# Kernel tuning notes

Hardware: AMD Instinct MI355X
Metric: run time of the kernel (lower is better)

## Reference

```python
import jax, jax.numpy as jnp
import numpy as np

N_NODES = 50000
N_EDGES = 800000
IN_DIM = 128
HIDDEN = 128


def setup_inputs() -> dict:
    key = jax.random.key(0)
    ks = jax.random.split(key, 6)
    x = jax.random.normal(ks[0], (N_NODES, IN_DIM), dtype=jnp.float32)
    edge_index = jax.random.randint(ks[1], (2, N_EDGES), 0, N_NODES, dtype=jnp.int32)
    W1 = jax.random.normal(ks[2], (IN_DIM, HIDDEN), dtype=jnp.float32) * 0.05
    b1 = jnp.zeros((HIDDEN,), dtype=jnp.float32)
    W2 = jax.random.normal(ks[3], (HIDDEN, HIDDEN), dtype=jnp.float32) * 0.05
    b2 = jnp.zeros((HIDDEN,), dtype=jnp.float32)
    return {"x": x, "edge_index": edge_index, "W1": W1, "b1": b1, "W2": W2, "b2": b2}


def _gcn_conv(x, W, b, src, dst, norm, n):
    # PyG GCNConv: linear transform, then normalized sum-aggregate, then bias.
    h = x @ W                                  # [N, H]
    msg = h[src] * norm[:, None]               # gather + scale  [E+N, H]
    out = jax.ops.segment_sum(msg, dst, num_segments=n)
    return out + b


def reference(x, edge_index, W1, b1, W2, b2):
    n = x.shape[0]
    # add self-loops (GCNConv default add_self_loops=True)
    loops = jnp.arange(n, dtype=edge_index.dtype)
    src = jnp.concatenate([edge_index[0], loops])
    dst = jnp.concatenate([edge_index[1], loops])
    # symmetric normalization: deg over destination nodes (edge_weight = 1)
    deg = jax.ops.segment_sum(jnp.ones(src.shape, dtype=x.dtype), dst, num_segments=n)
    dinv = jax.lax.rsqrt(deg)                  # deg >= 1 because of self-loops
    norm = dinv[src] * dinv[dst]               # [E+N]
    h = jax.nn.relu(_gcn_conv(x, W1, b1, src, dst, norm, n))
    return _gcn_conv(h, W2, b2, src, dst, norm, n)
```

## Files before the change

### kernel.cpp

```cpp
#include <hip/hip_runtime.h>

#define N_NODES 50000
#define N_EDGES 800000
#define DIM 128
#define CHUNK 4096
#define GRID 196
#define SEG_CAP 6144
#define GEMM_BLOCKS 391
#define GA 316
#define GB (GEMM_BLOCKS - GA)

typedef __attribute__((ext_vector_type(8))) short bf16x8;
typedef __attribute__((ext_vector_type(4))) float f32x4;


__device__ inline unsigned rne_bf16(float f) {
    unsigned u = __float_as_uint(f);
    return (u + 0x7FFFu + ((u >> 16) & 1u)) >> 16;
}
__device__ inline unsigned pk_bf16(float a, float b) {
    return rne_bf16(a) | (rne_bf16(b) << 16);
}
__device__ inline float bf_lo(unsigned u) { return __uint_as_float(u << 16); }
__device__ inline float bf_hi(unsigned u) { return __uint_as_float(u & 0xFFFF0000u); }


__device__ void fragw_build(const float* __restrict__ W, uint4* __restrict__ fh,
                            uint4* __restrict__ fl, int slot) {
    const int lane = slot & 63, tile = slot >> 6;
    const int c = tile >> 2, q = tile & 3;
    const int k0 = q * 32 + ((lane >> 4) << 3);
    const int col = c * 16 + (lane & 15);
    unsigned h[8], l[8];
#pragma unroll
    for (int j = 0; j < 8; ++j) {
        float w = W[(size_t)(k0 + j) * DIM + col];
        unsigned hb = rne_bf16(w);
        h[j] = hb;
        l[j] = rne_bf16(w - __uint_as_float(hb << 16));
    }
    uint4 uh, ul;
    uh.x = h[0] | (h[1] << 16); uh.y = h[2] | (h[3] << 16);
    uh.z = h[4] | (h[5] << 16); uh.w = h[6] | (h[7] << 16);
    ul.x = l[0] | (l[1] << 16); ul.y = l[2] | (l[3] << 16);
    ul.z = l[4] | (l[5] << 16); ul.w = l[6] | (l[7] << 16);
    fh[slot] = uh;
    fl[slot] = ul;
}


__global__ __launch_bounds__(256) void chunk_hist_fragw(const int* __restrict__ dst,
                                                        int* __restrict__ chist,
                                                        const float* __restrict__ W1,
                                                        const float* __restrict__ W2,
                                                        uint4* f1h, uint4* f1l,
                                                        uint4* f2h, uint4* f2l) {
    const int bid = blockIdx.x;
    if (bid < GRID) {
        __shared__ int hist[256];
        const int t = threadIdx.x;
        const int eb = bid * CHUNK;
        const int cnt = min(CHUNK, N_EDGES - eb);
        hist[t] = 0;
        __syncthreads();
        for (int i = t; i < cnt; i += 256)
            atomicAdd(&hist[dst[eb + i] >> 8], 1);
        __syncthreads();
        chist[bid * 256 + t] = hist[t];
    } else {
        const int b2 = bid - GRID;
        const int slot = (b2 & 7) * 256 + threadIdx.x;
        if (b2 < 8) fragw_build(W1, f1h, f1l, slot);
        else        fragw_build(W2, f2h, f2l, slot);
    }
}


__device__ void gemm_body(const float* __restrict__ X,
                          const uint4* __restrict__ fWh,
                          const uint4* __restrict__ fWl,
                          uint2* __restrict__ O, int gb, char* smem) {
    const int t = threadIdx.x;

    {
        uint4* s4 = (uint4*)smem;
        for (int i = t; i < 2048; i += 256) {
            s4[i] = fWh[i];
            s4[2048 + i] = fWl[i];
        }
    }
    __syncthreads();

    const int w = t >> 6, lane = t & 63;
    const int lrow = lane & 15, lgrp = lane >> 4;
    const int rbase = gb * 128;

    bf16x8 Ah[2][4], Al[2][4];
#pragma unroll
    for (int m = 0; m < 2; ++m) {
        const int r = rbase + w * 32 + m * 16 + lrow;
        const bool ok = (r < N_NODES);
        const float4* xp = (const float4*)(X + (size_t)r * DIM + lgrp * 8);
#pragma unroll
        for (int q = 0; q < 4; ++q) {
            float4 a0 = ok ? xp[q * 8]     : make_float4(0.f, 0.f, 0.f, 0.f);
            float4 a1 = ok ? xp[q * 8 + 1] : make_float4(0.f, 0.f, 0.f, 0.f);
            float f[8] = {a0.x, a0.y, a0.z, a0.w, a1.x, a1.y, a1.z, a1.w};
            bf16x8 hi, lo;
#pragma unroll
            for (int j = 0; j < 8; ++j) {
                unsigned hb = rne_bf16(f[j]);
                hi[j] = (short)hb;
                lo[j] = (short)rne_bf16(f[j] - __uint_as_float(hb << 16));
            }
            Ah[m][q] = hi;
            Al[m][q] = lo;
        }
    }

    f32x4 acc[2][8];
#pragma unroll
    for (int m = 0; m < 2; ++m)
#pragma unroll
        for (int c = 0; c < 8; ++c)
            acc[m][c] = (f32x4){0.f, 0.f, 0.f, 0.f};

    const bf16x8* Bh = (const bf16x8*)smem;
    const bf16x8* Bl = (const bf16x8*)(smem + 32768);
#pragma unroll
    for (int c = 0; c < 8; ++c) {
#pragma unroll
        for (int q = 0; q < 4; ++q) {
            bf16x8 bh = Bh[(c * 4 + q) * 64 + lane];
            bf16x8 bl = Bl[(c * 4 + q) * 64 + lane];
#pragma unroll
            for (int m = 0; m < 2; ++m) {
                acc[m][c] = __builtin_amdgcn_mfma_f32_16x16x32_bf16(Ah[m][q], bh, acc[m][c], 0, 0, 0);
                acc[m][c] = __builtin_amdgcn_mfma_f32_16x16x32_bf16(Al[m][q], bh, acc[m][c], 0, 0, 0);
                acc[m][c] = __builtin_amdgcn_mfma_f32_16x16x32_bf16(Ah[m][q], bl, acc[m][c], 0, 0, 0);
            }
        }
    }

    __syncthreads();
    float* Lf = (float*)smem;
#pragma unroll
    for (int m = 0; m < 2; ++m)
#pragma unroll
        for (int c = 0; c < 8; ++c)
#pragma unroll
            for (int rg = 0; rg < 4; ++rg)
                Lf[(w * 32 + m * 16 + lgrp * 4 + rg) * DIM + c * 16 + lrow] = acc[m][c][rg];
    __syncthreads();

    const float4* Lf4 = (const float4*)smem;
    for (int idx = t; idx < 4096; idx += 256) {
        const int row = idx >> 5, s = idx & 31;
        const int gr = rbase + row;
        if (gr < N_NODES) {
            float4 v = Lf4[idx];
            uint2 o;
            o.x = pk_bf16(v.x, v.y);
            o.y = pk_bf16(v.z, v.w);
            O[(size_t)gr * 32 + s] = o;
        }
    }
}


__device__ void sort_scatter_body(const int* __restrict__ src,
                                  const int* __restrict__ dst,
                                  const int* __restrict__ chist,
                                  unsigned* __restrict__ sorted,
                                  int* __restrict__ bbase_g,
                                  int bid, char* smem) {
    int* hist  = (int*)smem;
    int* sc    = hist + 256;
    int* lbase = sc + 256;
    int* lcur  = lbase + 256;
    int* gbase = lcur + 256;
    unsigned* sl = (unsigned*)(smem + 5 * 1024);

    const int t = threadIdx.x;
    const int eb = bid * CHUNK;
    const int cnt = min(CHUNK, N_EDGES - eb);

    int sum = 0, myoff = 0;
    for (int c = 0; c < GRID; ++c) {
        int v = chist[c * 256 + t];
        if (c == bid) myoff = sum;
        sum += v;
    }
    hist[t] = chist[bid * 256 + t];
    sc[t] = sum;
    __syncthreads();
    for (int off = 1; off < 256; off <<= 1) {
        int u = (t >= off) ? sc[t - off] : 0;
        __syncthreads();
        sc[t] += u;
        __syncthreads();
    }
    gbase[t] = (sc[t] - sum) + myoff;
    if (bid == 0) bbase_g[t] = sc[t] - sum;
    __syncthreads();

    sc[t] = hist[t];
    __syncthreads();
    for (int off = 1; off < 256; off <<= 1) {
        int u = (t >= off) ? sc[t - off] : 0;
        __syncthreads();
        sc[t] += u;
        __syncthreads();
    }
    int ex = sc[t] - hist[t];
    lbase[t] = ex;
    lcur[t] = ex;
    __syncthreads();

    for (int i = t; i < cnt; i += 256) {
        int s = src[eb + i], d = dst[eb + i];
        int b = d >> 8;
        int p = atomicAdd(&lcur[b], 1);
        sl[p] = ((unsigned)b << 24) | ((unsigned)(d & 255) << 16) | (unsigned)s;
    }
    __syncthreads();
    for (int i = t; i < cnt; i += 256) {
        unsigned rec = sl[i];
        int b = rec >> 24;
        sorted[gbase[b] + (i - lbase[b])] = rec;
    }
}


__device__ void csr_build_body(const unsigned* __restrict__ sorted,
                               const int* __restrict__ bbase,
                               int* __restrict__ rowptr,
                               float* __restrict__ dinv,
                               int* __restrict__ csr,
                               int k, char* smem) {
    int* hist = (int*)smem;
    int* sc   = hist + 256;
    int* lcur = sc + 256;
    int* seg  = (int*)(smem + 3 * 1024);

    const int t = threadIdx.x;
    const int base = bbase[k];
    const int cntk = ((k == 255) ? N_EDGES : bbase[k + 1]) - base;
    if (k == 0 && t == 0) rowptr[N_NODES] = N_EDGES;

    hist[t] = 0;
    __syncthreads();
    for (int i = t; i < cntk; i += 256)
        atomicAdd(&hist[(sorted[base + i] >> 16) & 255], 1);
    __syncthreads();

    const int node = (k << 8) + t;
    const int dv = hist[t];
    if (node < N_NODES) dinv[node] = rsqrtf((float)dv + 1.0f);

    sc[t] = dv;
    __syncthreads();
    for (int off = 1; off < 256; off <<= 1) {
        int u = (t >= off) ? sc[t - off] : 0;
        __syncthreads();
        sc[t] += u;
        __syncthreads();
    }
    int ex = sc[t] - dv;
    if (node < N_NODES) rowptr[node] = base + ex;
    lcur[t] = ex;
    __syncthreads();

    if (cntk <= SEG_CAP) {
        for (int i = t; i < cntk; i += 256) {
            unsigned rec = sorted[base + i];
            int p = atomicAdd(&lcur[(rec >> 16) & 255], 1);
            seg[p] = (int)(rec & 0xFFFFu);
        }
        __syncthreads();
        for (int i = t; i < cntk; i += 256)
            csr[base + i] = seg[i];
    } else {
        for (int i = t; i < cntk; i += 256) {
            unsigned rec = sorted[base + i];
            int p = atomicAdd(&lcur[(rec >> 16) & 255], 1);
            csr[base + p] = (int)(rec & 0xFFFFu);
        }
    }
}


__global__ __launch_bounds__(256, 2) void sort_gemm(const int* __restrict__ src,
                                                    const int* __restrict__ dst,
                                                    const int* __restrict__ chist,
                                                    unsigned* __restrict__ sorted,
                                                    int* __restrict__ bbase_g,
                                                    const float* __restrict__ X,
                                                    const uint4* __restrict__ fWh,
                                                    const uint4* __restrict__ fWl,
                                                    uint2* __restrict__ O) {
    __shared__ __align__(16) char smem[65536];
    if (blockIdx.x < GRID)
        sort_scatter_body(src, dst, chist, sorted, bbase_g, blockIdx.x, smem);
    else
        gemm_body(X, fWh, fWl, O, blockIdx.x - GRID, smem);
}

__global__ __launch_bounds__(256, 2) void csr_gemm(const unsigned* __restrict__ sorted,
                                                   const int* __restrict__ bbase,
                                                   int* __restrict__ rowptr,
                                                   float* __restrict__ dinv,
                                                   int* __restrict__ csr,
                                                   const float* __restrict__ X,
                                                   const uint4* __restrict__ fWh,
                                                   const uint4* __restrict__ fWl,
                                                   uint2* __restrict__ O) {
    __shared__ __align__(16) char smem[65536];
    if (blockIdx.x < GRID)
        csr_build_body(sorted, bbase, rowptr, dinv, csr, blockIdx.x, smem);
    else
        gemm_body(X, fWh, fWl, O, blockIdx.x - GRID + GA, smem);
}


__device__ inline float4 agg_node(int node, const uint2* __restrict__ H2,
                                  const int* __restrict__ rowptr,
                                  const int* __restrict__ csr,
                                  const float* __restrict__ dinv,
                                  const float4* __restrict__ b4, int relu) {
    const int lane = threadIdx.x & 63;
    const int half = lane >> 5;
    const int col  = lane & 31;

    const float dn = dinv[node];
    float4 acc = make_float4(0.f, 0.f, 0.f, 0.f);
    if (half == 0) {
        uint2 v = H2[(size_t)node * 32 + col];
        acc.x = dn * bf_lo(v.x); acc.y = dn * bf_hi(v.x);
        acc.z = dn * bf_lo(v.y); acc.w = dn * bf_hi(v.y);
    }

    int j = rowptr[node];
    const int end = rowptr[node + 1];

#define ACC(v, ds) do { \
        acc.x = fmaf((ds), bf_lo((v).x), acc.x); \
        acc.y = fmaf((ds), bf_hi((v).x), acc.y); \
        acc.z = fmaf((ds), bf_lo((v).y), acc.z); \
        acc.w = fmaf((ds), bf_hi((v).y), acc.w); } while (0)

    for (; j + 16 <= end; j += 16) {
        int s0 = csr[j +  0 + half], s1 = csr[j +  2 + half];
        int s2 = csr[j +  4 + half], s3 = csr[j +  6 + half];
        int s4 = csr[j +  8 + half], s5 = csr[j + 10 + half];
        int s6 = csr[j + 12 + half], s7 = csr[j + 14 + half];
        uint2 v0 = H2[(size_t)s0 * 32 + col]; float d0 = dinv[s0];
        uint2 v1 = H2[(size_t)s1 * 32 + col]; float d1 = dinv[s1];
        uint2 v2 = H2[(size_t)s2 * 32 + col]; float d2 = dinv[s2];
        uint2 v3 = H2[(size_t)s3 * 32 + col]; float d3 = dinv[s3];
        uint2 v4 = H2[(size_t)s4 * 32 + col]; float d4 = dinv[s4];
        uint2 v5 = H2[(size_t)s5 * 32 + col]; float d5 = dinv[s5];
        uint2 v6 = H2[(size_t)s6 * 32 + col]; float d6 = dinv[s6];
        uint2 v7 = H2[(size_t)s7 * 32 + col]; float d7 = dinv[s7];
        ACC(v0, d0); ACC(v1, d1); ACC(v2, d2); ACC(v3, d3);
        ACC(v4, d4); ACC(v5, d5); ACC(v6, d6); ACC(v7, d7);
    }
    if (j + 8 <= end) {
        int s0 = csr[j + half], s1 = csr[j + 2 + half];
        int s2 = csr[j + 4 + half], s3 = csr[j + 6 + half];
        uint2 v0 = H2[(size_t)s0 * 32 + col]; float d0 = dinv[s0];
        uint2 v1 = H2[(size_t)s1 * 32 + col]; float d1 = dinv[s1];
        uint2 v2 = H2[(size_t)s2 * 32 + col]; float d2 = dinv[s2];
        uint2 v3 = H2[(size_t)s3 * 32 + col]; float d3 = dinv[s3];
        ACC(v0, d0); ACC(v1, d1); ACC(v2, d2); ACC(v3, d3);
        j += 8;
    }
    if (j + 4 <= end) {
        int s0 = csr[j + half], s1 = csr[j + 2 + half];
        uint2 v0 = H2[(size_t)s0 * 32 + col]; float d0 = dinv[s0];
        uint2 v1 = H2[(size_t)s1 * 32 + col]; float d1 = dinv[s1];
        ACC(v0, d0); ACC(v1, d1);
        j += 4;
    }
    if (j + 2 <= end) {
        int s = csr[j + half];
        uint2 v = H2[(size_t)s * 32 + col]; float d0 = dinv[s];
        ACC(v, d0);
        j += 2;
    }
    if (j < end && half == 0) {
        int s = csr[j];
        uint2 v = H2[(size_t)s * 32 + col]; float d0 = dinv[s];
        ACC(v, d0);
    }
#undef ACC

    acc.x += __shfl_xor(acc.x, 32, 64);
    acc.y += __shfl_xor(acc.y, 32, 64);
    acc.z += __shfl_xor(acc.z, 32, 64);
    acc.w += __shfl_xor(acc.w, 32, 64);

    float4 o = make_float4(0.f, 0.f, 0.f, 0.f);
    if (half == 0) {
        float4 bb = b4[col];
        o.x = acc.x * dn + bb.x;
        o.y = acc.y * dn + bb.y;
        o.z = acc.z * dn + bb.z;
        o.w = acc.w * dn + bb.w;
        if (relu) {
            o.x = fmaxf(o.x, 0.f); o.y = fmaxf(o.y, 0.f);
            o.z = fmaxf(o.z, 0.f); o.w = fmaxf(o.w, 0.f);
        }
    }
    return o;
}


__global__ __launch_bounds__(256) void aggregate_h1(const uint2* __restrict__ H2,
                                                    const int* __restrict__ rowptr,
                                                    const int* __restrict__ csr,
                                                    const float* __restrict__ dinv,
                                                    const float4* __restrict__ b4,
                                                    uint2* __restrict__ h1h,
                                                    uint2* __restrict__ h1l) {
    int node = blockIdx.x * 4 + (threadIdx.x >> 6);
    if (node >= N_NODES) return;
    float4 o = agg_node(node, H2, rowptr, csr, dinv, b4, 1);
    const int lane = threadIdx.x & 63;
    if (lane < 32) {
        unsigned hx = rne_bf16(o.x), hy = rne_bf16(o.y);
        unsigned hz = rne_bf16(o.z), hw = rne_bf16(o.w);
        unsigned lx = rne_bf16(o.x - __uint_as_float(hx << 16));
        unsigned ly = rne_bf16(o.y - __uint_as_float(hy << 16));
        unsigned lz = rne_bf16(o.z - __uint_as_float(hz << 16));
        unsigned lw = rne_bf16(o.w - __uint_as_float(hw << 16));
        uint2 hv; hv.x = hx | (hy << 16); hv.y = hz | (hw << 16);
        uint2 lv; lv.x = lx | (ly << 16); lv.y = lz | (lw << 16);
        h1h[(size_t)node * 32 + lane] = hv;
        h1l[(size_t)node * 32 + lane] = lv;
    }
}


__global__ __launch_bounds__(256) void aggregate_out(const uint2* __restrict__ H2,
                                                     const int* __restrict__ rowptr,
                                                     const int* __restrict__ csr,
                                                     const float* __restrict__ dinv,
                                                     const float4* __restrict__ b4,
                                                     float4* __restrict__ out) {
    int node = blockIdx.x * 4 + (threadIdx.x >> 6);
    if (node >= N_NODES) return;
    float4 o = agg_node(node, H2, rowptr, csr, dinv, b4, 0);
    const int lane = threadIdx.x & 63;
    if (lane < 32) out[(size_t)node * 32 + lane] = o;
}


__global__ __launch_bounds__(256, 2) void gemm_xw2(const uint2* __restrict__ h1h,
                                                   const uint2* __restrict__ h1l,
                                                   const uint4* __restrict__ fWh,
                                                   const uint4* __restrict__ fWl,
                                                   uint2* __restrict__ O) {
    __shared__ __align__(16) char smem[65536];
    const int t = threadIdx.x;

    {
        uint4* s4 = (uint4*)smem;
        for (int i = t; i < 2048; i += 256) {
            s4[i] = fWh[i];
            s4[2048 + i] = fWl[i];
        }
    }
    __syncthreads();

    const int w = t >> 6, lane = t & 63;
    const int lrow = lane & 15, lgrp = lane >> 4;
    const int rbase = blockIdx.x * 128;

    bf16x8 Ah[2][4], Al[2][4];
    const bf16x8 zz = (bf16x8){0,0,0,0,0,0,0,0};
#pragma unroll
    for (int m = 0; m < 2; ++m) {
        const int r = rbase + w * 32 + m * 16 + lrow;
        const bool ok = (r < N_NODES);
        const uint2* ph = h1h + (size_t)r * 32 + lgrp * 2;
        const uint2* pl = h1l + (size_t)r * 32 + lgrp * 2;
#pragma unroll
        for (int q = 0; q < 4; ++q) {
            Ah[m][q] = ok ? *(const bf16x8*)(ph + q * 8) : zz;
            Al[m][q] = ok ? *(const bf16x8*)(pl + q * 8) : zz;
        }
    }

    f32x4 acc[2][8];
#pragma unroll
    for (int m = 0; m < 2; ++m)
#pragma unroll
        for (int c = 0; c < 8; ++c)
            acc[m][c] = (f32x4){0.f, 0.f, 0.f, 0.f};

    const bf16x8* Bh = (const bf16x8*)smem;
    const bf16x8* Bl = (const bf16x8*)(smem + 32768);
#pragma unroll
    for (int c = 0; c < 8; ++c) {
#pragma unroll
        for (int q = 0; q < 4; ++q) {
            bf16x8 bh = Bh[(c * 4 + q) * 64 + lane];
            bf16x8 bl = Bl[(c * 4 + q) * 64 + lane];
#pragma unroll
            for (int m = 0; m < 2; ++m) {
                acc[m][c] = __builtin_amdgcn_mfma_f32_16x16x32_bf16(Ah[m][q], bh, acc[m][c], 0, 0, 0);
                acc[m][c] = __builtin_amdgcn_mfma_f32_16x16x32_bf16(Al[m][q], bh, acc[m][c], 0, 0, 0);
                acc[m][c] = __builtin_amdgcn_mfma_f32_16x16x32_bf16(Ah[m][q], bl, acc[m][c], 0, 0, 0);
            }
        }
    }

    __syncthreads();
    float* Lf = (float*)smem;
#pragma unroll
    for (int m = 0; m < 2; ++m)
#pragma unroll
        for (int c = 0; c < 8; ++c)
#pragma unroll
            for (int rg = 0; rg < 4; ++rg)
                Lf[(w * 32 + m * 16 + lgrp * 4 + rg) * DIM + c * 16 + lrow] = acc[m][c][rg];
    __syncthreads();

    const float4* Lf4 = (const float4*)smem;
    for (int idx = t; idx < 4096; idx += 256) {
        const int row = idx >> 5, s = idx & 31;
        const int gr = rbase + row;
        if (gr < N_NODES) {
            float4 v = Lf4[idx];
            uint2 o;
            o.x = pk_bf16(v.x, v.y);
            o.y = pk_bf16(v.z, v.w);
            O[(size_t)gr * 32 + s] = o;
        }
    }
}


extern "C" void kernel_launch(void* const* d_in, const int* in_sizes, int n_in,
                              void* d_out, int out_size, void* d_ws, size_t ws_size,
                              hipStream_t stream) {
    const float* x  = (const float*)d_in[0];
    const int*   ei = (const int*)d_in[1];
    const float* W1 = (const float*)d_in[2];
    const float* b1 = (const float*)d_in[3];
    const float* W2 = (const float*)d_in[4];
    const float* b2 = (const float*)d_in[5];
    float* out = (float*)d_out;

    const int* src = ei;
    const int* dst = ei + N_EDGES;

    char* p = (char*)d_ws;
    int*      chist  = (int*)p;              p += GRID * 256 * 4;
    float*    dinv   = (float*)p;            p += ((N_NODES * 4 + 1023) & ~1023);
    int*      rowptr = (int*)p;              p += (((N_NODES + 1) * 4 + 1023) & ~1023);
    unsigned* sorted = (unsigned*)p;         p += ((N_EDGES * 4 + 1023) & ~1023);
    int*      csr    = (int*)p;              p += ((N_EDGES * 4 + 1023) & ~1023);
    int*      bbase  = (int*)p;              p += 1024;
    uint4*    f1h    = (uint4*)p;            p += 32768;
    uint4*    f1l    = (uint4*)p;            p += 32768;
    uint4*    f2h    = (uint4*)p;            p += 32768;
    uint4*    f2l    = (uint4*)p;            p += 32768;
    uint2*    hp     = (uint2*)p;            p += (size_t)N_NODES * DIM * 2;
    uint2*    h1h    = (uint2*)p;            p += (size_t)N_NODES * DIM * 2;
    uint2*    h1l    = (uint2*)p;            p += (size_t)N_NODES * DIM * 2;
    uint2*    hp2    = (uint2*)p;

    const int aggBlocks = (N_NODES + 3) / 4;

    chunk_hist_fragw<<<GRID + 16, 256, 0, stream>>>(dst, chist, W1, W2,
                                                    f1h, f1l, f2h, f2l);
    sort_gemm<<<GRID + GA, 256, 0, stream>>>(src, dst, chist, sorted, bbase,
                                             x, f1h, f1l, hp);
    csr_gemm<<<GRID + GB, 256, 0, stream>>>(sorted, bbase, rowptr, dinv, csr,
                                            x, f1h, f1l, hp);

    aggregate_h1<<<aggBlocks, 256, 0, stream>>>(hp, rowptr, csr, dinv,
                                                (const float4*)b1, h1h, h1l);

    gemm_xw2<<<GEMM_BLOCKS, 256, 0, stream>>>(h1h, h1l, f2h, f2l, hp2);

    aggregate_out<<<aggBlocks, 256, 0, stream>>>(hp2, rowptr, csr, dinv,
                                                 (const float4*)b2, (float4*)out);
}
```

Before: 209.1 us.

## Split aggregation feature dimension into four slices with 8-way edge parallelism

Each wavefront now handles one 32-column slice of a node's 128 features, with 8 lane groups processing different edges in parallel instead of 2 halves. The grid grows fourfold, with slice-major block ordering, so there are more waves in flight to hide gather latency and the tail handling becomes a single predicated step. The cost is four times the csr/dinv index reads, smaller 64-byte row segments per gather, and an extra shuffle reduction stage. Each slice pass may also lose L2 locality across the whole graph.

After: 296.4 us. 1.42x slower.

```diff
diff --git a/kernel.cpp b/kernel.cpp
--- a/kernel.cpp
+++ b/kernel.cpp
@@ -9,6 +9,7 @@
 #define GEMM_BLOCKS 391
 #define GA 316
 #define GB (GEMM_BLOCKS - GA)
+#define AGG_NB 12500
 
 typedef __attribute__((ext_vector_type(8))) short bf16x8;
 typedef __attribute__((ext_vector_type(4))) float f32x4;
@@ -323,19 +324,20 @@
 }
 
 
-__device__ inline float4 agg_node(int node, const uint2* __restrict__ H2,
-                                  const int* __restrict__ rowptr,
-                                  const int* __restrict__ csr,
-                                  const float* __restrict__ dinv,
-                                  const float4* __restrict__ b4, int relu) {
+__device__ inline float4 agg_node_slice(int node, int slice,
+                                        const uint2* __restrict__ H2,
+                                        const int* __restrict__ rowptr,
+                                        const int* __restrict__ csr,
+                                        const float* __restrict__ dinv,
+                                        const float4* __restrict__ b4, int relu) {
     const int lane = threadIdx.x & 63;
-    const int half = lane >> 5;
-    const int col  = lane & 31;
+    const int g    = lane >> 3;
+    const int idx  = slice * 8 + (lane & 7);
 
     const float dn = dinv[node];
     float4 acc = make_float4(0.f, 0.f, 0.f, 0.f);
-    if (half == 0) {
-        uint2 v = H2[(size_t)node * 32 + col];
+    if (g == 0) {
+        uint2 v = H2[(size_t)node * 32 + idx];
         acc.x = dn * bf_lo(v.x); acc.y = dn * bf_hi(v.x);
         acc.z = dn * bf_lo(v.y); acc.w = dn * bf_hi(v.y);
     }
@@ -350,59 +352,42 @@
         acc.w = fmaf((ds), bf_hi((v).y), acc.w); } while (0)
 
     for (; j + 16 <= end; j += 16) {
-        int s0 = csr[j +  0 + half], s1 = csr[j +  2 + half];
-        int s2 = csr[j +  4 + half], s3 = csr[j +  6 + half];
-        int s4 = csr[j +  8 + half], s5 = csr[j + 10 + half];
-        int s6 = csr[j + 12 + half], s7 = csr[j + 14 + half];
-        uint2 v0 = H2[(size_t)s0 * 32 + col]; float d0 = dinv[s0];
-        uint2 v1 = H2[(size_t)s1 * 32 + col]; float d1 = dinv[s1];
-        uint2 v2 = H2[(size_t)s2 * 32 + col]; float d2 = dinv[s2];
-        uint2 v3 = H2[(size_t)s3 * 32 + col]; float d3 = dinv[s3];
-        uint2 v4 = H2[(size_t)s4 * 32 + col]; float d4 = dinv[s4];
-        uint2 v5 = H2[(size_t)s5 * 32 + col]; float d5 = dinv[s5];
-        uint2 v6 = H2[(size_t)s6 * 32 + col]; float d6 = dinv[s6];
-        uint2 v7 = H2[(size_t)s7 * 32 + col]; float d7 = dinv[s7];
-        ACC(v0, d0); ACC(v1, d1); ACC(v2, d2); ACC(v3, d3);
-        ACC(v4, d4); ACC(v5, d5); ACC(v6, d6); ACC(v7, d7);
+        int s0 = csr[j + g];
+        int s1 = csr[j + 8 + g];
+        uint2 v0 = H2[(size_t)s0 * 32 + idx]; float d0 = dinv[s0];
+        uint2 v1 = H2[(size_t)s1 * 32 + idx]; float d1 = dinv[s1];
+        ACC(v0, d0); ACC(v1, d1);
     }
     if (j + 8 <= end) {
-        int s0 = csr[j + half], s1 = csr[j + 2 + half];
-        int s2 = csr[j + 4 + half], s3 = csr[j + 6 + half];
-        uint2 v0 = H2[(size_t)s0 * 32 + col]; float d0 = dinv[s0];
-        uint2 v1 = H2[(size_t)s1 * 32 + col]; float d1 = dinv[s1];
-        uint2 v2 = H2[(size_t)s2 * 32 + col]; float d2 = dinv[s2];
-        uint2 v3 = H2[(size_t)s3 * 32 + col]; float d3 = dinv[s3];
-        ACC(v0, d0); ACC(v1, d1); ACC(v2, d2); ACC(v3, d3);
+        int s = csr[j + g];
+        uint2 v = H2[(size_t)s * 32 + idx]; float d = dinv[s];
+        ACC(v, d);
         j += 8;
     }
-    if (j + 4 <= end) {
-        int s0 = csr[j + half], s1 = csr[j + 2 + half];
-        uint2 v0 = H2[(size_t)s0 * 32 + col]; float d0 = dinv[s0];
-        uint2 v1 = H2[(size_t)s1 * 32 + col]; float d1 = dinv[s1];
-        ACC(v0, d0); ACC(v1, d1);
-        j += 4;
-    }
-    if (j + 2 <= end) {
-        int s = csr[j + half];
-        uint2 v = H2[(size_t)s * 32 + col]; float d0 = dinv[s];
-        ACC(v, d0);
-        j += 2;
-    }
-    if (j < end && half == 0) {
-        int s = csr[j];
-        uint2 v = H2[(size_t)s * 32 + col]; float d0 = dinv[s];
-        ACC(v, d0);
+    const int rem = end - j;
+    if (g < rem) {
+        int s = csr[j + g];
+        uint2 v = H2[(size_t)s * 32 + idx]; float d = dinv[s];
+        ACC(v, d);
     }
 #undef ACC
 
+    acc.x += __shfl_xor(acc.x,  8, 64);
+    acc.y += __shfl_xor(acc.y,  8, 64);
+    acc.z += __shfl_xor(acc.z,  8, 64);
+    acc.w += __shfl_xor(acc.w,  8, 64);
+    acc.x += __shfl_xor(acc.x, 16, 64);
+    acc.y += __shfl_xor(acc.y, 16, 64);
+    acc.z += __shfl_xor(acc.z, 16, 64);
+    acc.w += __shfl_xor(acc.w, 16, 64);
     acc.x += __shfl_xor(acc.x, 32, 64);
     acc.y += __shfl_xor(acc.y, 32, 64);
     acc.z += __shfl_xor(acc.z, 32, 64);
     acc.w += __shfl_xor(acc.w, 32, 64);
 
     float4 o = make_float4(0.f, 0.f, 0.f, 0.f);
-    if (half == 0) {
-        float4 bb = b4[col];
+    if (lane < 8) {
+        float4 bb = b4[idx];
         o.x = acc.x * dn + bb.x;
         o.y = acc.y * dn + bb.y;
         o.z = acc.z * dn + bb.z;
@@ -423,11 +408,14 @@
                                                     const float4* __restrict__ b4,
                                                     uint2* __restrict__ h1h,
                                                     uint2* __restrict__ h1l) {
-    int node = blockIdx.x * 4 + (threadIdx.x >> 6);
+    const int slice = blockIdx.x / AGG_NB;
+    const int nb    = blockIdx.x % AGG_NB;
+    const int node  = nb * 4 + (threadIdx.x >> 6);
     if (node >= N_NODES) return;
-    float4 o = agg_node(node, H2, rowptr, csr, dinv, b4, 1);
+    float4 o = agg_node_slice(node, slice, H2, rowptr, csr, dinv, b4, 1);
     const int lane = threadIdx.x & 63;
-    if (lane < 32) {
+    if (lane < 8) {
+        const int idx = slice * 8 + lane;
         unsigned hx = rne_bf16(o.x), hy = rne_bf16(o.y);
         unsigned hz = rne_bf16(o.z), hw = rne_bf16(o.w);
         unsigned lx = rne_bf16(o.x - __uint_as_float(hx << 16));
@@ -436,8 +424,8 @@
         unsigned lw = rne_bf16(o.w - __uint_as_float(hw << 16));
         uint2 hv; hv.x = hx | (hy << 16); hv.y = hz | (hw << 16);
         uint2 lv; lv.x = lx | (ly << 16); lv.y = lz | (lw << 16);
-        h1h[(size_t)node * 32 + lane] = hv;
-        h1l[(size_t)node * 32 + lane] = lv;
+        h1h[(size_t)node * 32 + idx] = hv;
+        h1l[(size_t)node * 32 + idx] = lv;
     }
 }
 
@@ -448,11 +436,13 @@
                                                      const float* __restrict__ dinv,
                                                      const float4* __restrict__ b4,
                                                      float4* __restrict__ out) {
-    int node = blockIdx.x * 4 + (threadIdx.x >> 6);
+    const int slice = blockIdx.x / AGG_NB;
+    const int nb    = blockIdx.x % AGG_NB;
+    const int node  = nb * 4 + (threadIdx.x >> 6);
     if (node >= N_NODES) return;
-    float4 o = agg_node(node, H2, rowptr, csr, dinv, b4, 0);
+    float4 o = agg_node_slice(node, slice, H2, rowptr, csr, dinv, b4, 0);
     const int lane = threadIdx.x & 63;
-    if (lane < 32) out[(size_t)node * 32 + lane] = o;
+    if (lane < 8) out[(size_t)node * 32 + slice * 8 + lane] = o;
 }
 
 
@@ -572,8 +562,6 @@
     uint2*    h1l    = (uint2*)p;            p += (size_t)N_NODES * DIM * 2;
     uint2*    hp2    = (uint2*)p;
 
-    const int aggBlocks = (N_NODES + 3) / 4;
-
     chunk_hist_fragw<<<GRID + 16, 256, 0, stream>>>(dst, chist, W1, W2,
                                                     f1h, f1l, f2h, f2l);
     sort_gemm<<<GRID + GA, 256, 0, stream>>>(src, dst, chist, sorted, bbase,
@@ -581,11 +569,11 @@
     csr_gemm<<<GRID + GB, 256, 0, stream>>>(sorted, bbase, rowptr, dinv, csr,
                                             x, f1h, f1l, hp);
 
-    aggregate_h1<<<aggBlocks, 256, 0, stream>>>(hp, rowptr, csr, dinv,
-                                                (const float4*)b1, h1h, h1l);
+    aggregate_h1<<<4 * AGG_NB, 256, 0, stream>>>(hp, rowptr, csr, dinv,
+                                                 (const float4*)b1, h1h, h1l);
 
     gemm_xw2<<<GEMM_BLOCKS, 256, 0, stream>>>(h1h, h1l, f2h, f2l, hp2);
 
-    aggregate_out<<<aggBlocks, 256, 0, stream>>>(hp2, rowptr, csr, dinv,
-                                                 (const float4*)b2, (float4*)out);
-}
+    aggregate_out<<<4 * AGG_NB, 256, 0, stream>>>(hp2, rowptr, csr, dinv,
+                                                  (const float4*)b2, (float4*)out);
+}
```

## Widen aggregation gathers to 16-byte loads and prescale layer-2 input by dinv

Applied to the files above, without the earlier changes.

The aggregation kernels now have each wavefront split into four quarter-groups of 16 lanes that each load a full 128-bit slice per neighbor row, instead of two halves loading 64-bit slices. The layer-1 output is additionally multiplied by dinv before being stored, so the second aggregation drops its per-neighbor dinv gather and does plain adds. The aim is fewer, wider memory transactions and less random dinv traffic. The trade-off is an extra shuffle reduction stage and more registers per lane. Moving the dinv scale before the GEMM relies on it being linear, which holds but changes rounding slightly.

Result: faster. 203.5 us (-2.7%).

```diff
diff --git a/kernel.cpp b/kernel.cpp
--- a/kernel.cpp
+++ b/kernel.cpp
@@ -323,97 +323,17 @@
 }
 
 
-__device__ inline float4 agg_node(int node, const uint2* __restrict__ H2,
-                                  const int* __restrict__ rowptr,
-                                  const int* __restrict__ csr,
-                                  const float* __restrict__ dinv,
-                                  const float4* __restrict__ b4, int relu) {
-    const int lane = threadIdx.x & 63;
-    const int half = lane >> 5;
-    const int col  = lane & 31;
-
-    const float dn = dinv[node];
-    float4 acc = make_float4(0.f, 0.f, 0.f, 0.f);
-    if (half == 0) {
-        uint2 v = H2[(size_t)node * 32 + col];
-        acc.x = dn * bf_lo(v.x); acc.y = dn * bf_hi(v.x);
-        acc.z = dn * bf_lo(v.y); acc.w = dn * bf_hi(v.y);
-    }
-
-    int j = rowptr[node];
-    const int end = rowptr[node + 1];
-
-#define ACC(v, ds) do { \
-        acc.x = fmaf((ds), bf_lo((v).x), acc.x); \
-        acc.y = fmaf((ds), bf_hi((v).x), acc.y); \
-        acc.z = fmaf((ds), bf_lo((v).y), acc.z); \
-        acc.w = fmaf((ds), bf_hi((v).y), acc.w); } while (0)
-
-    for (; j + 16 <= end; j += 16) {
-        int s0 = csr[j +  0 + half], s1 = csr[j +  2 + half];
-        int s2 = csr[j +  4 + half], s3 = csr[j +  6 + half];
-        int s4 = csr[j +  8 + half], s5 = csr[j + 10 + half];
-        int s6 = csr[j + 12 + half], s7 = csr[j + 14 + half];
-        uint2 v0 = H2[(size_t)s0 * 32 + col]; float d0 = dinv[s0];
-        uint2 v1 = H2[(size_t)s1 * 32 + col]; float d1 = dinv[s1];
-        uint2 v2 = H2[(size_t)s2 * 32 + col]; float d2 = dinv[s2];
-        uint2 v3 = H2[(size_t)s3 * 32 + col]; float d3 = dinv[s3];
-        uint2 v4 = H2[(size_t)s4 * 32 + col]; float d4 = dinv[s4];
-        uint2 v5 = H2[(size_t)s5 * 32 + col]; float d5 = dinv[s5];
-        uint2 v6 = H2[(size_t)s6 * 32 + col]; float d6 = dinv[s6];
-        uint2 v7 = H2[(size_t)s7 * 32 + col]; float d7 = dinv[s7];
-        ACC(v0, d0); ACC(v1, d1); ACC(v2, d2); ACC(v3, d3);
-        ACC(v4, d4); ACC(v5, d5); ACC(v6, d6); ACC(v7, d7);
-    }
-    if (j + 8 <= end) {
-        int s0 = csr[j + half], s1 = csr[j + 2 + half];
-        int s2 = csr[j + 4 + half], s3 = csr[j + 6 + half];
-        uint2 v0 = H2[(size_t)s0 * 32 + col]; float d0 = dinv[s0];
-        uint2 v1 = H2[(size_t)s1 * 32 + col]; float d1 = dinv[s1];
-        uint2 v2 = H2[(size_t)s2 * 32 + col]; float d2 = dinv[s2];
-        uint2 v3 = H2[(size_t)s3 * 32 + col]; float d3 = dinv[s3];
-        ACC(v0, d0); ACC(v1, d1); ACC(v2, d2); ACC(v3, d3);
-        j += 8;
-    }
-    if (j + 4 <= end) {
-        int s0 = csr[j + half], s1 = csr[j + 2 + half];
-        uint2 v0 = H2[(size_t)s0 * 32 + col]; float d0 = dinv[s0];
-        uint2 v1 = H2[(size_t)s1 * 32 + col]; float d1 = dinv[s1];
-        ACC(v0, d0); ACC(v1, d1);
-        j += 4;
-    }
-    if (j + 2 <= end) {
-        int s = csr[j + half];
-        uint2 v = H2[(size_t)s * 32 + col]; float d0 = dinv[s];
-        ACC(v, d0);
-        j += 2;
-    }
-    if (j < end && half == 0) {
-        int s = csr[j];
-        uint2 v = H2[(size_t)s * 32 + col]; float d0 = dinv[s];
-        ACC(v, d0);
-    }
-#undef ACC
-
-    acc.x += __shfl_xor(acc.x, 32, 64);
-    acc.y += __shfl_xor(acc.y, 32, 64);
-    acc.z += __shfl_xor(acc.z, 32, 64);
-    acc.w += __shfl_xor(acc.w, 32, 64);
-
-    float4 o = make_float4(0.f, 0.f, 0.f, 0.f);
-    if (half == 0) {
-        float4 bb = b4[col];
-        o.x = acc.x * dn + bb.x;
-        o.y = acc.y * dn + bb.y;
-        o.z = acc.z * dn + bb.z;
-        o.w = acc.w * dn + bb.w;
-        if (relu) {
-            o.x = fmaxf(o.x, 0.f); o.y = fmaxf(o.y, 0.f);
-            o.z = fmaxf(o.z, 0.f); o.w = fmaxf(o.w, 0.f);
-        }
-    }
-    return o;
-}
+#define ACC8_D(v, d) do { \
+        a0 = fmaf((d), bf_lo((v).x), a0); a1 = fmaf((d), bf_hi((v).x), a1); \
+        a2 = fmaf((d), bf_lo((v).y), a2); a3 = fmaf((d), bf_hi((v).y), a3); \
+        a4 = fmaf((d), bf_lo((v).z), a4); a5 = fmaf((d), bf_hi((v).z), a5); \
+        a6 = fmaf((d), bf_lo((v).w), a6); a7 = fmaf((d), bf_hi((v).w), a7); } while (0)
+
+#define ACC8_P(v) do { \
+        a0 += bf_lo((v).x); a1 += bf_hi((v).x); \
+        a2 += bf_lo((v).y); a3 += bf_hi((v).y); \
+        a4 += bf_lo((v).z); a5 += bf_hi((v).z); \
+        a6 += bf_lo((v).w); a7 += bf_hi((v).w); } while (0)
 
 
 __global__ __launch_bounds__(256) void aggregate_h1(const uint2* __restrict__ H2,
@@ -421,23 +341,75 @@
                                                     const int* __restrict__ csr,
                                                     const float* __restrict__ dinv,
                                                     const float4* __restrict__ b4,
-                                                    uint2* __restrict__ h1h,
-                                                    uint2* __restrict__ h1l) {
-    int node = blockIdx.x * 4 + (threadIdx.x >> 6);
+                                                    uint4* __restrict__ h1h4,
+                                                    uint4* __restrict__ h1l4) {
+    const int node = blockIdx.x * 4 + (threadIdx.x >> 6);
     if (node >= N_NODES) return;
-    float4 o = agg_node(node, H2, rowptr, csr, dinv, b4, 1);
     const int lane = threadIdx.x & 63;
-    if (lane < 32) {
-        unsigned hx = rne_bf16(o.x), hy = rne_bf16(o.y);
-        unsigned hz = rne_bf16(o.z), hw = rne_bf16(o.w);
-        unsigned lx = rne_bf16(o.x - __uint_as_float(hx << 16));
-        unsigned ly = rne_bf16(o.y - __uint_as_float(hy << 16));
-        unsigned lz = rne_bf16(o.z - __uint_as_float(hz << 16));
-        unsigned lw = rne_bf16(o.w - __uint_as_float(hw << 16));
-        uint2 hv; hv.x = hx | (hy << 16); hv.y = hz | (hw << 16);
-        uint2 lv; lv.x = lx | (ly << 16); lv.y = lz | (lw << 16);
-        h1h[(size_t)node * 32 + lane] = hv;
-        h1l[(size_t)node * 32 + lane] = lv;
+    const int q = lane >> 4, l16 = lane & 15;
+    const uint4* H4 = (const uint4*)H2;
+
+    const float dn = dinv[node];
+    float a0 = 0.f, a1 = 0.f, a2 = 0.f, a3 = 0.f,
+          a4 = 0.f, a5 = 0.f, a6 = 0.f, a7 = 0.f;
+    if (q == 0) {
+        uint4 v = H4[(size_t)node * 16 + l16];
+        ACC8_D(v, dn);
+    }
+
+    int j = rowptr[node];
+    const int end = rowptr[node + 1];
+    for (; j + 8 <= end; j += 8) {
+        int s0 = csr[j + q], s1 = csr[j + 4 + q];
+        uint4 v0 = H4[(size_t)s0 * 16 + l16]; float d0 = dinv[s0];
+        uint4 v1 = H4[(size_t)s1 * 16 + l16]; float d1 = dinv[s1];
+        ACC8_D(v0, d0); ACC8_D(v1, d1);
+    }
+    if (j + 4 <= end) {
+        int s = csr[j + q];
+        uint4 v = H4[(size_t)s * 16 + l16]; float d = dinv[s];
+        ACC8_D(v, d);
+        j += 4;
+    }
+    if (q < end - j) {
+        int s = csr[j + q];
+        uint4 v = H4[(size_t)s * 16 + l16]; float d = dinv[s];
+        ACC8_D(v, d);
+    }
+
+    a0 += __shfl_xor(a0, 16, 64); a1 += __shfl_xor(a1, 16, 64);
+    a2 += __shfl_xor(a2, 16, 64); a3 += __shfl_xor(a3, 16, 64);
+    a4 += __shfl_xor(a4, 16, 64); a5 += __shfl_xor(a5, 16, 64);
+    a6 += __shfl_xor(a6, 16, 64); a7 += __shfl_xor(a7, 16, 64);
+    a0 += __shfl_xor(a0, 32, 64); a1 += __shfl_xor(a1, 32, 64);
+    a2 += __shfl_xor(a2, 32, 64); a3 += __shfl_xor(a3, 32, 64);
+    a4 += __shfl_xor(a4, 32, 64); a5 += __shfl_xor(a5, 32, 64);
+    a6 += __shfl_xor(a6, 32, 64); a7 += __shfl_xor(a7, 32, 64);
+
+    if (lane < 16) {
+        float4 bbA = b4[l16 * 2], bbB = b4[l16 * 2 + 1];
+        float o0 = fmaxf(a0 * dn + bbA.x, 0.f), o1 = fmaxf(a1 * dn + bbA.y, 0.f);
+        float o2 = fmaxf(a2 * dn + bbA.z, 0.f), o3 = fmaxf(a3 * dn + bbA.w, 0.f);
+        float o4 = fmaxf(a4 * dn + bbB.x, 0.f), o5 = fmaxf(a5 * dn + bbB.y, 0.f);
+        float o6 = fmaxf(a6 * dn + bbB.z, 0.f), o7 = fmaxf(a7 * dn + bbB.w, 0.f);
+        o0 *= dn; o1 *= dn; o2 *= dn; o3 *= dn;
+        o4 *= dn; o5 *= dn; o6 *= dn; o7 *= dn;
+        unsigned h0 = rne_bf16(o0), h1 = rne_bf16(o1), h2 = rne_bf16(o2), h3 = rne_bf16(o3);
+        unsigned h4 = rne_bf16(o4), h5 = rne_bf16(o5), h6 = rne_bf16(o6), h7 = rne_bf16(o7);
+        uint4 hv;
+        hv.x = h0 | (h1 << 16); hv.y = h2 | (h3 << 16);
+        hv.z = h4 | (h5 << 16); hv.w = h6 | (h7 << 16);
+        uint4 lv;
+        lv.x = rne_bf16(o0 - __uint_as_float(h0 << 16)) |
+               (rne_bf16(o1 - __uint_as_float(h1 << 16)) << 16);
+        lv.y = rne_bf16(o2 - __uint_as_float(h2 << 16)) |
+               (rne_bf16(o3 - __uint_as_float(h3 << 16)) << 16);
+        lv.z = rne_bf16(o4 - __uint_as_float(h4 << 16)) |
+               (rne_bf16(o5 - __uint_as_float(h5 << 16)) << 16);
+        lv.w = rne_bf16(o6 - __uint_as_float(h6 << 16)) |
+               (rne_bf16(o7 - __uint_as_float(h7 << 16)) << 16);
+        h1h4[(size_t)node * 16 + l16] = hv;
+        h1l4[(size_t)node * 16 + l16] = lv;
     }
 }
 
@@ -448,11 +420,59 @@
                                                      const float* __restrict__ dinv,
                                                      const float4* __restrict__ b4,
                                                      float4* __restrict__ out) {
-    int node = blockIdx.x * 4 + (threadIdx.x >> 6);
+    const int node = blockIdx.x * 4 + (threadIdx.x >> 6);
     if (node >= N_NODES) return;
-    float4 o = agg_node(node, H2, rowptr, csr, dinv, b4, 0);
     const int lane = threadIdx.x & 63;
-    if (lane < 32) out[(size_t)node * 32 + lane] = o;
+    const int q = lane >> 4, l16 = lane & 15;
+    const uint4* H4 = (const uint4*)H2;
+
+    float a0 = 0.f, a1 = 0.f, a2 = 0.f, a3 = 0.f,
+          a4 = 0.f, a5 = 0.f, a6 = 0.f, a7 = 0.f;
+    if (q == 0) {
+        uint4 v = H4[(size_t)node * 16 + l16];
+        ACC8_P(v);
+    }
+
+    int j = rowptr[node];
+    const int end = rowptr[node + 1];
+    for (; j + 8 <= end; j += 8) {
+        int s0 = csr[j + q], s1 = csr[j + 4 + q];
+        uint4 v0 = H4[(size_t)s0 * 16 + l16];
+        uint4 v1 = H4[(size_t)s1 * 16 + l16];
+        ACC8_P(v0); ACC8_P(v1);
+    }
+    if (j + 4 <= end) {
+        int s = csr[j + q];
+        uint4 v = H4[(size_t)s * 16 + l16];
+        ACC8_P(v);
+        j += 4;
+    }
+    if (q < end - j) {
+        int s = csr[j + q];
+        uint4 v = H4[(size_t)s * 16 + l16];
+        ACC8_P(v);
+    }
+
+    a0 += __shfl_xor(a0, 16, 64); a1 += __shfl_xor(a1, 16, 64);
+    a2 += __shfl_xor(a2, 16, 64); a3 += __shfl_xor(a3, 16, 64);
+    a4 += __shfl_xor(a4, 16, 64); a5 += __shfl_xor(a5, 16, 64);
+    a6 += __shfl_xor(a6, 16, 64); a7 += __shfl_xor(a7, 16, 64);
+    a0 += __shfl_xor(a0, 32, 64); a1 += __shfl_xor(a1, 32, 64);
+    a2 += __shfl_xor(a2, 32, 64); a3 += __shfl_xor(a3, 32, 64);
+    a4 += __shfl_xor(a4, 32, 64); a5 += __shfl_xor(a5, 32, 64);
+    a6 += __shfl_xor(a6, 32, 64); a7 += __shfl_xor(a7, 32, 64);
+
+    if (lane < 16) {
+        const float dn = dinv[node];
+        float4 bbA = b4[l16 * 2], bbB = b4[l16 * 2 + 1];
+        float4 oA, oB;
+        oA.x = a0 * dn + bbA.x; oA.y = a1 * dn + bbA.y;
+        oA.z = a2 * dn + bbA.z; oA.w = a3 * dn + bbA.w;
+        oB.x = a4 * dn + bbB.x; oB.y = a5 * dn + bbB.y;
+        oB.z = a6 * dn + bbB.z; oB.w = a7 * dn + bbB.w;
+        out[(size_t)node * 32 + l16 * 2]     = oA;
+        out[(size_t)node * 32 + l16 * 2 + 1] = oB;
+    }
 }
 
 
@@ -582,7 +602,8 @@
                                             x, f1h, f1l, hp);
 
     aggregate_h1<<<aggBlocks, 256, 0, stream>>>(hp, rowptr, csr, dinv,
-                                                (const float4*)b1, h1h, h1l);
+                                                (const float4*)b1,
+                                                (uint4*)h1h, (uint4*)h1l);
 
     gemm_xw2<<<GEMM_BLOCKS, 256, 0, stream>>>(h1h, h1l, f2h, f2l, hp2);
 
```
